# Performance work log

Measured on AMD Instinct MI355X. Metric: run time of the kernel, lower is better.

## Reference

```python
import jax, jax.numpy as jnp
import numpy as np

BATCH = 8192
MAX_ATOMS = 512  # angles_max_length


def setup_inputs() -> dict:
    key = jax.random.key(0)
    k1, k2, k3 = jax.random.split(key, 3)
    inp = jax.random.normal(k1, (BATCH, 3 * MAX_ATOMS), dtype=jnp.float32)
    tgt = jax.random.normal(k2, (BATCH, 3 * MAX_ATOMS), dtype=jnp.float32)
    num_atoms = jax.random.randint(k3, (BATCH,), 0, MAX_ATOMS, dtype=jnp.int64)
    num_atoms = jnp.maximum(num_atoms, 16)  # avoid degenerate tiny structures
    return {"input": inp, "target": tgt, "num_atoms": num_atoms}


def _kabsch_rmsd(inp, tgt, num_atoms):
    B = inp.shape[0]
    N = inp.shape[1] // 3
    src = inp.reshape(B, N, 3)
    dst = tgt.reshape(B, N, 3)
    # mask out padding atoms
    mask = (jnp.arange(N)[None, :] < num_atoms[:, None])[..., None]  # [B,N,1]
    n = num_atoms.astype(inp.dtype)[:, None, None]                   # [B,1,1]
    src = jnp.where(mask, src, 0.0)
    dst = jnp.where(dst.dtype.type(0) == 0, jnp.where(mask, dst, 0.0), dst)
    # center on masked centroid, re-zero padding
    src_c = jnp.where(mask, src - jnp.sum(src, axis=1, keepdims=True) / n, 0.0)
    dst_c = jnp.where(mask, dst - jnp.sum(dst, axis=1, keepdims=True) / n, 0.0)
    # 3x3 correlation matrices
    R = jnp.einsum("bni,bnj->bij", src_c, dst_c)  # [B,3,3]
    U, S, Vt = jnp.linalg.svd(R)
    d = jnp.sign(jnp.linalg.det(U) * jnp.linalg.det(Vt))  # chirality correction
    trace_opt = S[:, 0] + S[:, 1] + d * S[:, 2]
    sq = jnp.sum(src_c * src_c, axis=(1, 2)) + jnp.sum(dst_c * dst_c, axis=(1, 2))
    na = num_atoms.astype(inp.dtype)
    msd = (sq - 2.0 * trace_opt) / na
    return jnp.sqrt(jnp.clip(msd, 0.0))


def reference(input, target, num_atoms):
    return _kabsch_rmsd(input, target, num_atoms)
```

## Files before the change

### kernel.cpp

```cpp
#include <hip/hip_runtime.h>
#include <math.h>

#define NATOMS 512
#define TPB 256

__global__ __launch_bounds__(TPB) void kabsch_rmsd_kernel(
    const float* __restrict__ inp,
    const float* __restrict__ tgt,
    const int* __restrict__ num_atoms,
    float* __restrict__ out)
{
    const int b = blockIdx.x;
    const int t = threadIdx.x;
    const int na = num_atoms[b];

    const float* src = inp + (size_t)b * (3 * NATOMS);
    const float* dst = tgt + (size_t)b * (3 * NATOMS);

    const float2* s2 = (const float2*)src + 3 * t;
    const float2* d2 = (const float2*)dst + 3 * t;
    float2 sA = s2[0], sB = s2[1], sC = s2[2];
    float2 dA = d2[0], dB = d2[1], dC = d2[2];

    float s0x = sA.x, s0y = sA.y, s0z = sB.x;
    float s1x = sB.y, s1y = sC.x, s1z = sC.y;
    float d0x = dA.x, d0y = dA.y, d0z = dB.x;
    float d1x = dB.y, d1y = dC.x, d1z = dC.y;

    const int a0 = 2 * t, a1 = 2 * t + 1;
    if (a0 >= na) { s0x = s0y = s0z = 0.f; d0x = d0y = d0z = 0.f; }
    if (a1 >= na) { s1x = s1y = s1z = 0.f; d1x = d1y = d1z = 0.f; }

    float v[16];
    v[0]  = s0x * d0x + s1x * d1x;
    v[1]  = s0x * d0y + s1x * d1y;
    v[2]  = s0x * d0z + s1x * d1z;
    v[3]  = s0y * d0x + s1y * d1x;
    v[4]  = s0y * d0y + s1y * d1y;
    v[5]  = s0y * d0z + s1y * d1z;
    v[6]  = s0z * d0x + s1z * d1x;
    v[7]  = s0z * d0y + s1z * d1y;
    v[8]  = s0z * d0z + s1z * d1z;
    v[9]  = s0x + s1x;
    v[10] = s0y + s1y;
    v[11] = s0z + s1z;
    v[12] = d0x + d1x;
    v[13] = d0y + d1y;
    v[14] = d0z + d1z;
    v[15] = s0x * s0x + s0y * s0y + s0z * s0z
          + s1x * s1x + s1y * s1y + s1z * s1z
          + d0x * d0x + d0y * d0y + d0z * d0z
          + d1x * d1x + d1y * d1y + d1z * d1z;

    #pragma unroll
    for (int i = 0; i < 16; ++i) {
        #pragma unroll
        for (int off = 32; off > 0; off >>= 1) {
            v[i] += __shfl_down(v[i], off);
        }
    }

    __shared__ float red[4][16];
    const int wave = t >> 6;
    const int lane = t & 63;
    if (lane == 0) {
        #pragma unroll
        for (int i = 0; i < 16; ++i) red[wave][i] = v[i];
    }
    __syncthreads();

    if (t == 0) {
        double acc[16];
        #pragma unroll
        for (int i = 0; i < 16; ++i) {
            acc[i] = (double)red[0][i] + (double)red[1][i]
                   + (double)red[2][i] + (double)red[3][i];
        }
        const double n = (double)na;
        const double sx = acc[9],  sy = acc[10], sz = acc[11];
        const double tx = acc[12], ty = acc[13], tz = acc[14];

        double R[3][3];
        R[0][0] = acc[0] - sx * tx / n;
        R[0][1] = acc[1] - sx * ty / n;
        R[0][2] = acc[2] - sx * tz / n;
        R[1][0] = acc[3] - sy * tx / n;
        R[1][1] = acc[4] - sy * ty / n;
        R[1][2] = acc[5] - sy * tz / n;
        R[2][0] = acc[6] - sz * tx / n;
        R[2][1] = acc[7] - sz * ty / n;
        R[2][2] = acc[8] - sz * tz / n;

        const double sq = acc[15] - (sx * sx + sy * sy + sz * sz
                                   + tx * tx + ty * ty + tz * tz) / n;

        const double detR =
            R[0][0] * (R[1][1] * R[2][2] - R[1][2] * R[2][1])
          - R[0][1] * (R[1][0] * R[2][2] - R[1][2] * R[2][0])
          + R[0][2] * (R[1][0] * R[2][1] - R[1][1] * R[2][0]);

        double A00 = R[0][0]*R[0][0] + R[1][0]*R[1][0] + R[2][0]*R[2][0];
        double A11 = R[0][1]*R[0][1] + R[1][1]*R[1][1] + R[2][1]*R[2][1];
        double A22 = R[0][2]*R[0][2] + R[1][2]*R[1][2] + R[2][2]*R[2][2];
        double A01 = R[0][0]*R[0][1] + R[1][0]*R[1][1] + R[2][0]*R[2][1];
        double A02 = R[0][0]*R[0][2] + R[1][0]*R[1][2] + R[2][0]*R[2][2];
        double A12 = R[0][1]*R[0][2] + R[1][1]*R[1][2] + R[2][1]*R[2][2];

        double e0, e1, e2;
        const double p1 = A01*A01 + A02*A02 + A12*A12;
        if (p1 < 1e-30) {
            e0 = A00; e1 = A11; e2 = A22;
            double tmp;
            if (e0 < e1) { tmp = e0; e0 = e1; e1 = tmp; }
            if (e1 < e2) { tmp = e1; e1 = e2; e2 = tmp; }
            if (e0 < e1) { tmp = e0; e0 = e1; e1 = tmp; }
        } else {
            const double q  = (A00 + A11 + A22) / 3.0;
            const double b00 = A00 - q, b11 = A11 - q, b22 = A22 - q;
            const double p2 = b00*b00 + b11*b11 + b22*b22 + 2.0 * p1;
            const double p  = sqrt(p2 / 6.0);
            const double ip = 1.0 / p;
            const double B00 = b00*ip, B11 = b11*ip, B22 = b22*ip;
            const double B01 = A01*ip, B02 = A02*ip, B12 = A12*ip;
            double r = 0.5 * (B00 * (B11 * B22 - B12 * B12)
                            - B01 * (B01 * B22 - B12 * B02)
                            + B02 * (B01 * B12 - B11 * B02));
            if (r < -1.0) r = -1.0;
            if (r >  1.0) r =  1.0;
            const double phi = acos(r) / 3.0;
            e0 = q + 2.0 * p * cos(phi);
            e2 = q + 2.0 * p * cos(phi + 2.0943951023931953);
            e1 = 3.0 * q - e0 - e2;
        }

        const double S0 = sqrt(e0 > 0.0 ? e0 : 0.0);
        const double S1 = sqrt(e1 > 0.0 ? e1 : 0.0);
        const double S2 = sqrt(e2 > 0.0 ? e2 : 0.0);
        const double dsgn = (detR > 0.0) ? 1.0 : ((detR < 0.0) ? -1.0 : 0.0);
        const double trace_opt = S0 + S1 + dsgn * S2;

        double msd = (sq - 2.0 * trace_opt) / n;
        if (msd < 0.0) msd = 0.0;
        out[b] = (float)sqrt(msd);
    }
}

extern "C" void kernel_launch(void* const* d_in, const int* in_sizes, int n_in,
                              void* d_out, int out_size, void* d_ws, size_t ws_size,
                              hipStream_t stream) {
    const float* inp = (const float*)d_in[0];
    const float* tgt = (const float*)d_in[1];
    const int* num_atoms = (const int*)d_in[2];
    float* out = (float*)d_out;

    const int B = in_sizes[0] / (3 * NATOMS);
    kabsch_rmsd_kernel<<<B, TPB, 0, stream>>>(inp, tgt, num_atoms, out);
}
```

Measured before the change: 134.0 us.

## Map one wavefront per batch row with float4 loads and wave-only reduction

Each 64-lane wavefront now handles a whole structure, so a 256-thread block covers four batch rows. Every lane loads 8 atoms through six float4 loads per array and accumulates sums in registers. The reduction is a wave-level xor shuffle with no shared memory or __syncthreads, and lane 0 of each wave runs the double-precision eigen solve. This removes block-level synchronisation and the serial tail of one thread per block, in exchange for more registers per thread and a quarter as many blocks.

```diff
diff --git a/kernel.cpp b/kernel.cpp
--- a/kernel.cpp
+++ b/kernel.cpp
@@ -3,96 +3,80 @@
 
 #define NATOMS 512
 #define TPB 256
+#define WPB 4
 
 __global__ __launch_bounds__(TPB) void kabsch_rmsd_kernel(
     const float* __restrict__ inp,
     const float* __restrict__ tgt,
     const int* __restrict__ num_atoms,
-    float* __restrict__ out)
+    float* __restrict__ out,
+    int B)
 {
-    const int b = blockIdx.x;
-    const int t = threadIdx.x;
+    const int wave = threadIdx.x >> 6;
+    const int lane = threadIdx.x & 63;
+    const int b = blockIdx.x * WPB + wave;
+    if (b >= B) return;
+
     const int na = num_atoms[b];
 
-    const float* src = inp + (size_t)b * (3 * NATOMS);
-    const float* dst = tgt + (size_t)b * (3 * NATOMS);
+    const float4* s4 = (const float4*)(inp + (size_t)b * (3 * NATOMS)) + 6 * lane;
+    const float4* d4 = (const float4*)(tgt + (size_t)b * (3 * NATOMS)) + 6 * lane;
 
-    const float2* s2 = (const float2*)src + 3 * t;
-    const float2* d2 = (const float2*)dst + 3 * t;
-    float2 sA = s2[0], sB = s2[1], sC = s2[2];
-    float2 dA = d2[0], dB = d2[1], dC = d2[2];
-
-    float s0x = sA.x, s0y = sA.y, s0z = sB.x;
-    float s1x = sB.y, s1y = sC.x, s1z = sC.y;
-    float d0x = dA.x, d0y = dA.y, d0z = dB.x;
-    float d1x = dB.y, d1y = dC.x, d1z = dC.y;
-
-    const int a0 = 2 * t, a1 = 2 * t + 1;
-    if (a0 >= na) { s0x = s0y = s0z = 0.f; d0x = d0y = d0z = 0.f; }
-    if (a1 >= na) { s1x = s1y = s1z = 0.f; d1x = d1y = d1z = 0.f; }
+    union U { float4 q[6]; float f[24]; };
+    U S, D;
+    #pragma unroll
+    for (int i = 0; i < 6; ++i) S.q[i] = s4[i];
+    #pragma unroll
+    for (int i = 0; i < 6; ++i) D.q[i] = d4[i];
 
     float v[16];
-    v[0]  = s0x * d0x + s1x * d1x;
-    v[1]  = s0x * d0y + s1x * d1y;
-    v[2]  = s0x * d0z + s1x * d1z;
-    v[3]  = s0y * d0x + s1y * d1x;
-    v[4]  = s0y * d0y + s1y * d1y;
-    v[5]  = s0y * d0z + s1y * d1z;
-    v[6]  = s0z * d0x + s1z * d1x;
-    v[7]  = s0z * d0y + s1z * d1y;
-    v[8]  = s0z * d0z + s1z * d1z;
-    v[9]  = s0x + s1x;
-    v[10] = s0y + s1y;
-    v[11] = s0z + s1z;
-    v[12] = d0x + d1x;
-    v[13] = d0y + d1y;
-    v[14] = d0z + d1z;
-    v[15] = s0x * s0x + s0y * s0y + s0z * s0z
-          + s1x * s1x + s1y * s1y + s1z * s1z
-          + d0x * d0x + d0y * d0y + d0z * d0z
-          + d1x * d1x + d1y * d1y + d1z * d1z;
+    #pragma unroll
+    for (int i = 0; i < 16; ++i) v[i] = 0.f;
+
+    const int base = lane * 8;
+    #pragma unroll
+    for (int k = 0; k < 8; ++k) {
+        const float m = (base + k < na) ? 1.f : 0.f;
+        const float sx = S.f[3 * k]     * m;
+        const float sy = S.f[3 * k + 1] * m;
+        const float sz = S.f[3 * k + 2] * m;
+        const float dx = D.f[3 * k]     * m;
+        const float dy = D.f[3 * k + 1] * m;
+        const float dz = D.f[3 * k + 2] * m;
+        v[0]  += sx * dx;  v[1]  += sx * dy;  v[2]  += sx * dz;
+        v[3]  += sy * dx;  v[4]  += sy * dy;  v[5]  += sy * dz;
+        v[6]  += sz * dx;  v[7]  += sz * dy;  v[8]  += sz * dz;
+        v[9]  += sx;  v[10] += sy;  v[11] += sz;
+        v[12] += dx;  v[13] += dy;  v[14] += dz;
+        v[15] += sx * sx + sy * sy + sz * sz + dx * dx + dy * dy + dz * dz;
+    }
 
     #pragma unroll
     for (int i = 0; i < 16; ++i) {
         #pragma unroll
-        for (int off = 32; off > 0; off >>= 1) {
-            v[i] += __shfl_down(v[i], off);
+        for (int mask = 32; mask > 0; mask >>= 1) {
+            v[i] += __shfl_xor(v[i], mask);
         }
     }
 
-    __shared__ float red[4][16];
-    const int wave = t >> 6;
-    const int lane = t & 63;
     if (lane == 0) {
-        #pragma unroll
-        for (int i = 0; i < 16; ++i) red[wave][i] = v[i];
-    }
-    __syncthreads();
-
-    if (t == 0) {
-        double acc[16];
-        #pragma unroll
-        for (int i = 0; i < 16; ++i) {
-            acc[i] = (double)red[0][i] + (double)red[1][i]
-                   + (double)red[2][i] + (double)red[3][i];
-        }
         const double n = (double)na;
-        const double sx = acc[9],  sy = acc[10], sz = acc[11];
-        const double tx = acc[12], ty = acc[13], tz = acc[14];
+        const double sx = (double)v[9],  sy = (double)v[10], sz = (double)v[11];
+        const double tx = (double)v[12], ty = (double)v[13], tz = (double)v[14];
 
         double R[3][3];
-        R[0][0] = acc[0] - sx * tx / n;
-        R[0][1] = acc[1] - sx * ty / n;
-        R[0][2] = acc[2] - sx * tz / n;
-        R[1][0] = acc[3] - sy * tx / n;
-        R[1][1] = acc[4] - sy * ty / n;
-        R[1][2] = acc[5] - sy * tz / n;
-        R[2][0] = acc[6] - sz * tx / n;
-        R[2][1] = acc[7] - sz * ty / n;
-        R[2][2] = acc[8] - sz * tz / n;
+        R[0][0] = (double)v[0] - sx * tx / n;
+        R[0][1] = (double)v[1] - sx * ty / n;
+        R[0][2] = (double)v[2] - sx * tz / n;
+        R[1][0] = (double)v[3] - sy * tx / n;
+        R[1][1] = (double)v[4] - sy * ty / n;
+        R[1][2] = (double)v[5] - sy * tz / n;
+        R[2][0] = (double)v[6] - sz * tx / n;
+        R[2][1] = (double)v[7] - sz * ty / n;
+        R[2][2] = (double)v[8] - sz * tz / n;
 
-        const double sq = acc[15] - (sx * sx + sy * sy + sz * sz
-                                   + tx * tx + ty * ty + tz * tz) / n;
+        const double sq = (double)v[15] - (sx * sx + sy * sy + sz * sz
+                                         + tx * tx + ty * ty + tz * tz) / n;
 
         const double detR =
             R[0][0] * (R[1][1] * R[2][2] - R[1][2] * R[2][1])
@@ -154,5 +138,6 @@
     float* out = (float*)d_out;
 
     const int B = in_sizes[0] / (3 * NATOMS);
-    kabsch_rmsd_kernel<<<B, TPB, 0, stream>>>(inp, tgt, num_atoms, out);
+    const int blocks = (B + WPB - 1) / WPB;
+    kabsch_rmsd_kernel<<<blocks, TPB, 0, stream>>>(inp, tgt, num_atoms, out, B);
 }
```

Result: faster. 124.4 us (-7.2%).
